# Performance work log

Hardware: AMD Instinct MI355X
Metric: run time of the kernel (lower is better)

The kernel has to match this reference:

```python
import jax, jax.numpy as jnp
import numpy as np

B, C_IN, C_OUT, L = 16, 128, 128, 1024
DK, DV, H = 32, 32, 8
SCALE = DK ** (-0.5)


def setup_inputs() -> dict:
    key = jax.random.key(0)
    ks = jax.random.split(key, 7)
    qkv_dim = H * (2 * DK + DV)
    # Conv1d with kernel_size=1 == per-position linear; store weights as (out, in)
    return {
        "x": jax.random.normal(ks[0], (B, C_IN, L), dtype=jnp.float32),
        "w_qkv": jax.random.normal(ks[1], (qkv_dim, C_IN), dtype=jnp.float32) * (C_IN ** -0.5),
        "b_qkv": jax.random.normal(ks[2], (qkv_dim,), dtype=jnp.float32) * 0.02,
        "w_o": jax.random.normal(ks[3], (C_OUT, H * DV), dtype=jnp.float32) * ((H * DV) ** -0.5),
        "b_o": jax.random.normal(ks[4], (C_OUT,), dtype=jnp.float32) * 0.02,
        "w_res": jax.random.normal(ks[5], (C_OUT, C_IN), dtype=jnp.float32) * (C_IN ** -0.5),
        "b_res": jax.random.normal(ks[6], (C_OUT,), dtype=jnp.float32) * 0.02,
    }


def reference(x, w_qkv, b_qkv, w_o, b_o, w_res, b_res):
    batch, _, seq = x.shape
    # qkv projection (1x1 conv): (B, H*(2dk+dv), L)
    qkv = jnp.einsum("oc,bcl->bol", w_qkv, x) + b_qkv[:, None]
    qkv = qkv.reshape(batch, H, 2 * DK + DV, seq)
    q = qkv[:, :, :DK]                 # (B, H, dk, L)
    k = qkv[:, :, DK:2 * DK]           # (B, H, dk, L)
    v = qkv[:, :, 2 * DK:]             # (B, H, dv, L)
    # logits = scale * q^T k : (B, H, L, L)
    logits = SCALE * jnp.einsum("bhds,bhdt->bhst", q, k)
    weights = jax.nn.softmax(logits, axis=-1)
    # z_i = (weights @ v^T)^T : (B, H, dv, L)
    z = jnp.einsum("bhst,bhdt->bhds", weights, v)
    z = z.reshape(batch, H * DV, seq)
    out = jnp.einsum("oc,bcl->bol", w_o, z) + b_o[:, None]
    out = out + jnp.einsum("oc,bcl->bol", w_res, x) + b_res[:, None]
    return out
```

## Files before the change

kernel.cpp:

```cpp
#include <hip/hip_runtime.h>

#define B_    16
#define L_    1024
#define H_    8
#define QSCALE 0.25510940349191965f

typedef __attribute__((ext_vector_type(8))) short bf16x8;
typedef __attribute__((ext_vector_type(4))) float f32x4;
typedef unsigned short u16t;

__device__ inline u16t f2bf(float f) {
    unsigned u = __float_as_uint(f);
    u = (u + 0x7FFF + ((u >> 16) & 1)) >> 16;
    return (u16t)u;
}
__device__ inline unsigned f2bf_pk(float a, float b) {
    unsigned ua = __float_as_uint(a);
    unsigned ub = __float_as_uint(b);
    ua = (ua + 0x7FFF + ((ua >> 16) & 1)) >> 16;
    ub = (ub + 0x7FFF + ((ub >> 16) & 1)) >> 16;
    return ua | (ub << 16);
}
__device__ inline uint2 f2bf_pk4(float a, float b, float c, float d) {
    uint2 u; u.x = f2bf_pk(a, b); u.y = f2bf_pk(c, d); return u;
}
__device__ inline unsigned trunc_pk(float f0, float f1) {
    return __builtin_amdgcn_perm(__float_as_uint(f1), __float_as_uint(f0), 0x07060302u);
}
__device__ inline void async16(const u16t* g, u16t* l) {
    __builtin_amdgcn_global_load_lds(
        (const __attribute__((address_space(1))) unsigned int*)g,
        (__attribute__((address_space(3))) unsigned int*)l, 16, 0, 0);
}

__global__ __launch_bounds__(256) void prep_kernel(
    const float* __restrict__ x, u16t* __restrict__ xbT)
{
    __shared__ u16t T[64][144];
    const int tid = threadIdx.x;
    const int b = blockIdx.y, l0 = blockIdx.x * 64;
#pragma unroll
    for (int i = 0; i < 8; i++) {
        const int c = i * 16 + (tid >> 4);
        const int l = (tid & 15) * 4;
        const float4 v = *(const float4*)(x + ((long)b * 128 + c) * 1024 + l0 + l);
        T[l + 0][c] = f2bf(v.x);
        T[l + 1][c] = f2bf(v.y);
        T[l + 2][c] = f2bf(v.z);
        T[l + 3][c] = f2bf(v.w);
    }
    __syncthreads();
#pragma unroll
    for (int i = 0; i < 4; i++) {
        const int l  = i * 16 + (tid >> 4);
        const int c0 = (tid & 15) * 8;
        *(uint4*)(xbT + ((long)b * 1024 + l0 + l) * 128 + c0) = *(const uint4*)&T[l][c0];
    }
}

__global__ __launch_bounds__(256) void qkv_gemm_kernel(
    const float* __restrict__ w_qkv, const u16t* __restrict__ xbT,
    const float* __restrict__ b_qkv,
    u16t* __restrict__ qT, u16t* __restrict__ kF, u16t* __restrict__ vF)
{
    __shared__ __align__(16) u16t Ws[96 * 136];

    const int lblk = blockIdx.x * 128;
    const int bh = blockIdx.y;
    const int b = bh >> 3, h = bh & 7;
    const int tid = threadIdx.x, lane = tid & 63, wv = tid >> 6;
    const int l15 = lane & 15, quad = lane >> 4;
    const int lw = lblk + wv * 32;

    {
        const float* wsrc = w_qkv + (long)h * 96 * 128;
#pragma unroll
        for (int it = 0; it < 12; it++) {
            const int g = tid * 4 + it * 1024;
            const int row = g >> 7, col = g & 127;
            const float4 w = *(const float4*)(wsrc + g);
            *(uint2*)&Ws[row * 136 + col] = f2bf_pk4(w.x, w.y, w.z, w.w);
        }
    }

    bf16x8 bfr[4][2];
    {
        const u16t* xr0 = xbT + ((long)b * 1024 + lw + l15) * 128 + quad * 8;
        const u16t* xr1 = xr0 + 16 * 128;
#pragma unroll
        for (int ks = 0; ks < 4; ks++) {
            bfr[ks][0] = *(const bf16x8*)(xr0 + ks * 32);
            bfr[ks][1] = *(const bf16x8*)(xr1 + ks * 32);
        }
    }
    __syncthreads();

    f32x4 acc[6][2];
#pragma unroll
    for (int mi = 0; mi < 6; mi++)
#pragma unroll
        for (int ni = 0; ni < 2; ni++) acc[mi][ni] = (f32x4)0.f;

#pragma unroll
    for (int ks = 0; ks < 4; ks++) {
#pragma unroll
        for (int mi = 0; mi < 6; mi++) {
            const bf16x8 af = *(const bf16x8*)&Ws[(mi * 16 + l15) * 136 + ks * 32 + quad * 8];
            acc[mi][0] = __builtin_amdgcn_mfma_f32_16x16x32_bf16(af, bfr[ks][0], acc[mi][0], 0, 0, 0);
            acc[mi][1] = __builtin_amdgcn_mfma_f32_16x16x32_bf16(af, bfr[ks][1], acc[mi][1], 0, 0, 0);
        }
    }

    const long bh_ = bh;
#pragma unroll
    for (int mi = 0; mi < 6; mi++) {
        float bias[4];
#pragma unroll
        for (int r = 0; r < 4; r++) bias[r] = b_qkv[h * 96 + mi * 16 + quad * 4 + r];
#pragma unroll
        for (int ni = 0; ni < 2; ni++) {
            const int l = lw + ni * 16 + l15;
            const f32x4 a = acc[mi][ni];
            if (mi < 2) {
                const uint2 u = f2bf_pk4((a[0] + bias[0]) * QSCALE, (a[1] + bias[1]) * QSCALE,
                                         (a[2] + bias[2]) * QSCALE, (a[3] + bias[3]) * QSCALE);
                *(uint2*)(qT + (bh_ * 1024 + l) * 32 + mi * 16 + quad * 4) = u;
            } else if (mi < 4) {
                const int t = l, c = t >> 6, tl = t & 63;
                const int qd = (mi - 2) * 2 + (quad >> 1);
                const uint2 u = f2bf_pk4(a[0] + bias[0], a[1] + bias[1],
                                         a[2] + bias[2], a[3] + bias[3]);
                *(uint2*)(kF + (bh_ * 16 + c) * 2048 + qd * 512 + tl * 8 + (quad & 1) * 4) = u;
            } else {
                const int t = l, c = t >> 6, tq = (t >> 3) & 7, j = t & 7;
                u16t* vb = vF + (bh_ * 16 + c) * 2048 + tq * 256 + j;
#pragma unroll
                for (int r = 0; r < 4; r++)
                    vb[((mi - 4) * 16 + quad * 4 + r) * 8] = f2bf(a[r] + bias[r]);
            }
        }
    }
}

__global__ __launch_bounds__(512) void attn_kernel9(
    const u16t* __restrict__ qT, const u16t* __restrict__ kF,
    const u16t* __restrict__ vF, u16t* __restrict__ zT)
{
    __shared__ __align__(16) u16t Ks[2][2048];
    __shared__ __align__(16) u16t Vs[2][2048];
    __shared__ __align__(16) u16t Ps[8][2][2][16][40];

    const int bh = blockIdx.x;
    const int b = bh >> 3, h = bh & 7;
    const int sblk = blockIdx.y * 256;
    const int tid = threadIdx.x, lane = tid & 63, wv = tid >> 6;
    const int l15 = lane & 15, quad = lane >> 4;

    const int sw = sblk + wv * 32;
    bf16x8 qf[2];
    qf[0] = *(const bf16x8*)(qT + ((long)bh * 1024 + sw + l15) * 32 + quad * 8);
    qf[1] = *(const bf16x8*)(qT + ((long)bh * 1024 + sw + 16 + l15) * 32 + quad * 8);

    const u16t* kg = kF + (long)bh * 32768;
    const u16t* vg = vF + (long)bh * 32768;

    if (tid < 256) async16(kg + tid * 8, &Ks[0][tid * 8]);
    else           async16(vg + (tid - 256) * 8, &Vs[0][(tid - 256) * 8]);

    f32x4 zacc[2][2];
#pragma unroll
    for (int a = 0; a < 2; a++)
#pragma unroll
        for (int c = 0; c < 2; c++) zacc[a][c] = (f32x4)0.f;
    f32x4 lacc4[2] = {(f32x4)0.f, (f32x4)0.f};

    for (int c = 0; c < 16; ++c) {
        const int buf = c & 1;
        __syncthreads();
        if (c < 15) {
            const int o = (c + 1) * 2048;
            if (tid < 256) async16(kg + o + tid * 8, &Ks[buf ^ 1][tid * 8]);
            else           async16(vg + o + (tid - 256) * 8, &Vs[buf ^ 1][(tid - 256) * 8]);
        }

        bf16x8 kf[4];
#pragma unroll
        for (int tg = 0; tg < 4; tg++)
            kf[tg] = *(const bf16x8*)&Ks[buf][quad * 512 + (tg * 16 + l15) * 8];

#pragma unroll
        for (int st = 0; st < 2; st++) {
#pragma unroll
            for (int tg = 0; tg < 4; tg++) {
                const f32x4 sv = __builtin_amdgcn_mfma_f32_16x16x32_bf16(kf[tg], qf[st], (f32x4)0.f, 0, 0, 0);
                f32x4 ev;
#pragma unroll
                for (int i = 0; i < 4; i++) ev[i] = __builtin_amdgcn_exp2f(sv[i]);
                lacc4[st] += ev;
                uint2 u;
                u.x = trunc_pk(ev[0], ev[1]);
                u.y = trunc_pk(ev[2], ev[3]);
                *(uint2*)&Ps[wv][st][tg >> 1][l15][(tg & 1) * 16 + quad * 4] = u;
            }
        }

#pragma unroll
        for (int st = 0; st < 2; st++) {
#pragma unroll
            for (int tt = 0; tt < 2; tt++) {
                const bf16x8 pf  = *(const bf16x8*)&Ps[wv][st][tt][l15][quad * 8];
                const bf16x8 vf0 = *(const bf16x8*)&Vs[buf][(tt * 4 + quad) * 256 + l15 * 8];
                const bf16x8 vf1 = *(const bf16x8*)&Vs[buf][(tt * 4 + quad) * 256 + (16 + l15) * 8];
                zacc[st][0] = __builtin_amdgcn_mfma_f32_16x16x32_bf16(vf0, pf, zacc[st][0], 0, 0, 0);
                zacc[st][1] = __builtin_amdgcn_mfma_f32_16x16x32_bf16(vf1, pf, zacc[st][1], 0, 0, 0);
            }
        }
    }

#pragma unroll
    for (int st = 0; st < 2; st++) {
        float lf = (lacc4[st][0] + lacc4[st][1]) + (lacc4[st][2] + lacc4[st][3]);
        lf += __shfl_xor(lf, 16);
        lf += __shfl_xor(lf, 32);
        const float rl = 1.f / lf;
        const int s = sblk + wv * 32 + st * 16 + l15;
        u16t* zrow = zT + ((long)b * 1024 + s) * 256 + h * 32;
        const uint2 u0 = f2bf_pk4(zacc[st][0][0] * rl, zacc[st][0][1] * rl,
                                  zacc[st][0][2] * rl, zacc[st][0][3] * rl);
        *(uint2*)(zrow + quad * 4) = u0;
        const uint2 u1 = f2bf_pk4(zacc[st][1][0] * rl, zacc[st][1][1] * rl,
                                  zacc[st][1][2] * rl, zacc[st][1][3] * rl);
        *(uint2*)(zrow + 16 + quad * 4) = u1;
    }
}

__global__ __launch_bounds__(256) void out_gemm_kernel(
    const float* __restrict__ w_o, const float* __restrict__ w_res,
    const u16t* __restrict__ zT, const u16t* __restrict__ xbT,
    const float* __restrict__ b_o, const float* __restrict__ b_res,
    float* __restrict__ out)
{
    __shared__ __align__(16) u16t Wo[64 * 264];
    __shared__ __align__(16) u16t Wr[64 * 136];

    const int lblk = blockIdx.x * 32, oblk = blockIdx.y * 64, b = blockIdx.z;
    const int tid = threadIdx.x, lane = tid & 63, wv = tid >> 6;
    const int wm = wv >> 1, wn = wv & 1;
    const int l15 = lane & 15, quad = lane >> 4;
    const int ow = oblk + wm * 32;
    const int lw = lblk + wn * 16;

#pragma unroll
    for (int it = 0; it < 16; it++) {
        const int g = tid * 4 + it * 1024;
        const int row = g >> 8, col = g & 255;
        const float4 w = *(const float4*)(w_o + (long)(oblk + row) * 256 + col);
        *(uint2*)&Wo[row * 264 + col] = f2bf_pk4(w.x, w.y, w.z, w.w);
    }
#pragma unroll
    for (int it = 0; it < 8; it++) {
        const int g = tid * 4 + it * 1024;
        const int row = g >> 7, col = g & 127;
        const float4 w = *(const float4*)(w_res + (long)(oblk + row) * 128 + col);
        *(uint2*)&Wr[row * 136 + col] = f2bf_pk4(w.x, w.y, w.z, w.w);
    }

    bf16x8 bfz[8], bfx[4];
    {
        const u16t* zrow = zT + ((long)b * 1024 + lw + l15) * 256 + quad * 8;
        const u16t* xrow = xbT + ((long)b * 1024 + lw + l15) * 128 + quad * 8;
#pragma unroll
        for (int ks = 0; ks < 8; ks++) bfz[ks] = *(const bf16x8*)(zrow + ks * 32);
#pragma unroll
        for (int ks = 0; ks < 4; ks++) bfx[ks] = *(const bf16x8*)(xrow + ks * 32);
    }
    __syncthreads();

    f32x4 acc0 = (f32x4)0.f, acc1 = (f32x4)0.f;

#pragma unroll
    for (int ks = 0; ks < 8; ks++) {
        const bf16x8 af0 = *(const bf16x8*)&Wo[(wm * 32 + l15) * 264 + ks * 32 + quad * 8];
        const bf16x8 af1 = *(const bf16x8*)&Wo[(wm * 32 + 16 + l15) * 264 + ks * 32 + quad * 8];
        acc0 = __builtin_amdgcn_mfma_f32_16x16x32_bf16(af0, bfz[ks], acc0, 0, 0, 0);
        acc1 = __builtin_amdgcn_mfma_f32_16x16x32_bf16(af1, bfz[ks], acc1, 0, 0, 0);
    }
#pragma unroll
    for (int ks = 0; ks < 4; ks++) {
        const bf16x8 af0 = *(const bf16x8*)&Wr[(wm * 32 + l15) * 136 + ks * 32 + quad * 8];
        const bf16x8 af1 = *(const bf16x8*)&Wr[(wm * 32 + 16 + l15) * 136 + ks * 32 + quad * 8];
        acc0 = __builtin_amdgcn_mfma_f32_16x16x32_bf16(af0, bfx[ks], acc0, 0, 0, 0);
        acc1 = __builtin_amdgcn_mfma_f32_16x16x32_bf16(af1, bfx[ks], acc1, 0, 0, 0);
    }

    const int lcol = lw + l15;
#pragma unroll
    for (int mi = 0; mi < 2; mi++) {
        const f32x4 a = (mi == 0) ? acc0 : acc1;
#pragma unroll
        for (int r = 0; r < 4; r++) {
            const int o = ow + mi * 16 + quad * 4 + r;
            out[((long)b * 128 + o) * 1024 + lcol] = a[r] + b_o[o] + b_res[o];
        }
    }
}

extern "C" void kernel_launch(void* const* d_in, const int* in_sizes, int n_in,
                              void* d_out, int out_size, void* d_ws, size_t ws_size,
                              hipStream_t stream)
{
    const float* x     = (const float*)d_in[0];
    const float* w_qkv = (const float*)d_in[1];
    const float* b_qkv = (const float*)d_in[2];
    const float* w_o   = (const float*)d_in[3];
    const float* b_o   = (const float*)d_in[4];
    const float* w_res = (const float*)d_in[5];
    const float* b_res = (const float*)d_in[6];
    float* out = (float*)d_out;

    u16t* xbT = (u16t*)d_ws;
    u16t* qT  = xbT + (size_t)2097152;
    u16t* kF  = qT  + (size_t)4194304;
    u16t* vF  = kF  + (size_t)4194304;
    u16t* zT  = vF  + (size_t)4194304;

    prep_kernel<<<dim3(16, 16), 256, 0, stream>>>(x, xbT);
    qkv_gemm_kernel<<<dim3(8, 128), 256, 0, stream>>>(w_qkv, xbT, b_qkv, qT, kF, vF);
    attn_kernel9<<<dim3(128, 4), 512, 0, stream>>>(qT, kF, vF, zT);
    out_gemm_kernel<<<dim3(32, 2, 16), 256, 0, stream>>>(w_o, w_res, zT, xbT, b_o, b_res, out);
}
```

Measured before the change: 127.0 us.

## Fuse x transpose into QKV GEMM and double attention K/V chunk size

Removes the separate prep kernel. The QKV GEMM now reads fp32 x directly, transposes and converts it into shared memory, and has the h==0 blocks write the bf16 xbT copy the output GEMM still needs. Weights are loaded from global and converted to bf16 per MFMA instead of being staged in LDS. The attention kernel uses 128-key chunks (8 iterations instead of 16), which halves the number of barriers, and the K/V layouts written by the QKV kernel change to match. In exchange, x is reconverted by all 8 head blocks, weight loads become uncoalesced global reads inside the inner loop, and LDS use grows.

```diff
diff --git a/kernel.cpp b/kernel.cpp
--- a/kernel.cpp
+++ b/kernel.cpp
@@ -33,37 +33,13 @@
         (__attribute__((address_space(3))) unsigned int*)l, 16, 0, 0);
 }
 
-__global__ __launch_bounds__(256) void prep_kernel(
-    const float* __restrict__ x, u16t* __restrict__ xbT)
+__global__ __launch_bounds__(256) void qkv_gemm_kernel(
+    const float* __restrict__ w_qkv, const float* __restrict__ x,
+    const float* __restrict__ b_qkv,
+    u16t* __restrict__ qT, u16t* __restrict__ kF, u16t* __restrict__ vF,
+    u16t* __restrict__ xbT)
 {
-    __shared__ u16t T[64][144];
-    const int tid = threadIdx.x;
-    const int b = blockIdx.y, l0 = blockIdx.x * 64;
-#pragma unroll
-    for (int i = 0; i < 8; i++) {
-        const int c = i * 16 + (tid >> 4);
-        const int l = (tid & 15) * 4;
-        const float4 v = *(const float4*)(x + ((long)b * 128 + c) * 1024 + l0 + l);
-        T[l + 0][c] = f2bf(v.x);
-        T[l + 1][c] = f2bf(v.y);
-        T[l + 2][c] = f2bf(v.z);
-        T[l + 3][c] = f2bf(v.w);
-    }
-    __syncthreads();
-#pragma unroll
-    for (int i = 0; i < 4; i++) {
-        const int l  = i * 16 + (tid >> 4);
-        const int c0 = (tid & 15) * 8;
-        *(uint4*)(xbT + ((long)b * 1024 + l0 + l) * 128 + c0) = *(const uint4*)&T[l][c0];
-    }
-}
-
-__global__ __launch_bounds__(256) void qkv_gemm_kernel(
-    const float* __restrict__ w_qkv, const u16t* __restrict__ xbT,
-    const float* __restrict__ b_qkv,
-    u16t* __restrict__ qT, u16t* __restrict__ kF, u16t* __restrict__ vF)
-{
-    __shared__ __align__(16) u16t Ws[96 * 136];
+    __shared__ __align__(16) u16t Xs[128][136];
 
     const int lblk = blockIdx.x * 128;
     const int bh = blockIdx.y;
@@ -72,42 +48,57 @@
     const int l15 = lane & 15, quad = lane >> 4;
     const int lw = lblk + wv * 32;
 
-    {
-        const float* wsrc = w_qkv + (long)h * 96 * 128;
-#pragma unroll
-        for (int it = 0; it < 12; it++) {
-            const int g = tid * 4 + it * 1024;
-            const int row = g >> 7, col = g & 127;
-            const float4 w = *(const float4*)(wsrc + g);
-            *(uint2*)&Ws[row * 136 + col] = f2bf_pk4(w.x, w.y, w.z, w.w);
-        }
-    }
-
-    bf16x8 bfr[4][2];
-    {
-        const u16t* xr0 = xbT + ((long)b * 1024 + lw + l15) * 128 + quad * 8;
-        const u16t* xr1 = xr0 + 16 * 128;
-#pragma unroll
-        for (int ks = 0; ks < 4; ks++) {
-            bfr[ks][0] = *(const bf16x8*)(xr0 + ks * 32);
-            bfr[ks][1] = *(const bf16x8*)(xr1 + ks * 32);
-        }
+#pragma unroll
+    for (int i = 0; i < 8; i++) {
+        const int c  = i * 16 + (tid >> 4);
+        const int l8 = (tid & 15) * 8;
+        const float* xr = x + ((long)b * 128 + c) * 1024 + lblk + l8;
+        const float4 va = *(const float4*)(xr);
+        const float4 vb = *(const float4*)(xr + 4);
+        Xs[l8 + 0][c] = f2bf(va.x);
+        Xs[l8 + 1][c] = f2bf(va.y);
+        Xs[l8 + 2][c] = f2bf(va.z);
+        Xs[l8 + 3][c] = f2bf(va.w);
+        Xs[l8 + 4][c] = f2bf(vb.x);
+        Xs[l8 + 5][c] = f2bf(vb.y);
+        Xs[l8 + 6][c] = f2bf(vb.z);
+        Xs[l8 + 7][c] = f2bf(vb.w);
     }
     __syncthreads();
 
+    if (h == 0) {
+#pragma unroll
+        for (int i = 0; i < 8; i++) {
+            const int l  = i * 16 + (tid >> 4);
+            const int c0 = (tid & 15) * 8;
+            *(uint4*)(xbT + ((long)b * 1024 + lblk + l) * 128 + c0) = *(const uint4*)&Xs[l][c0];
+        }
+    }
+
     f32x4 acc[6][2];
 #pragma unroll
     for (int mi = 0; mi < 6; mi++)
 #pragma unroll
         for (int ni = 0; ni < 2; ni++) acc[mi][ni] = (f32x4)0.f;
 
+    const float* wbase = w_qkv + ((long)h * 96 + l15) * 128 + quad * 8;
+
 #pragma unroll
     for (int ks = 0; ks < 4; ks++) {
+        const bf16x8 bf0 = *(const bf16x8*)&Xs[wv * 32 + l15][ks * 32 + quad * 8];
+        const bf16x8 bf1 = *(const bf16x8*)&Xs[wv * 32 + 16 + l15][ks * 32 + quad * 8];
 #pragma unroll
         for (int mi = 0; mi < 6; mi++) {
-            const bf16x8 af = *(const bf16x8*)&Ws[(mi * 16 + l15) * 136 + ks * 32 + quad * 8];
-            acc[mi][0] = __builtin_amdgcn_mfma_f32_16x16x32_bf16(af, bfr[ks][0], acc[mi][0], 0, 0, 0);
-            acc[mi][1] = __builtin_amdgcn_mfma_f32_16x16x32_bf16(af, bfr[ks][1], acc[mi][1], 0, 0, 0);
+            const float* wr = wbase + mi * 16 * 128 + ks * 32;
+            const float4 wa = *(const float4*)(wr);
+            const float4 wb = *(const float4*)(wr + 4);
+            union { uint4 u; bf16x8 v; } af;
+            af.u.x = f2bf_pk(wa.x, wa.y);
+            af.u.y = f2bf_pk(wa.z, wa.w);
+            af.u.z = f2bf_pk(wb.x, wb.y);
+            af.u.w = f2bf_pk(wb.z, wb.w);
+            acc[mi][0] = __builtin_amdgcn_mfma_f32_16x16x32_bf16(af.v, bf0, acc[mi][0], 0, 0, 0);
+            acc[mi][1] = __builtin_amdgcn_mfma_f32_16x16x32_bf16(af.v, bf1, acc[mi][1], 0, 0, 0);
         }
     }
 
@@ -126,14 +117,14 @@
                                          (a[2] + bias[2]) * QSCALE, (a[3] + bias[3]) * QSCALE);
                 *(uint2*)(qT + (bh_ * 1024 + l) * 32 + mi * 16 + quad * 4) = u;
             } else if (mi < 4) {
-                const int t = l, c = t >> 6, tl = t & 63;
+                const int t = l, c = t >> 7, tl = t & 127;
                 const int qd = (mi - 2) * 2 + (quad >> 1);
                 const uint2 u = f2bf_pk4(a[0] + bias[0], a[1] + bias[1],
                                          a[2] + bias[2], a[3] + bias[3]);
-                *(uint2*)(kF + (bh_ * 16 + c) * 2048 + qd * 512 + tl * 8 + (quad & 1) * 4) = u;
+                *(uint2*)(kF + (bh_ * 8 + c) * 4096 + qd * 1024 + tl * 8 + (quad & 1) * 4) = u;
             } else {
-                const int t = l, c = t >> 6, tq = (t >> 3) & 7, j = t & 7;
-                u16t* vb = vF + (bh_ * 16 + c) * 2048 + tq * 256 + j;
+                const int t = l, c = t >> 7, tq = (t >> 3) & 15, j = t & 7;
+                u16t* vb = vF + (bh_ * 8 + c) * 4096 + tq * 256 + j;
 #pragma unroll
                 for (int r = 0; r < 4; r++)
                     vb[((mi - 4) * 16 + quad * 4 + r) * 8] = f2bf(a[r] + bias[r]);
@@ -142,12 +133,12 @@
     }
 }
 
-__global__ __launch_bounds__(512) void attn_kernel9(
+__global__ __launch_bounds__(512) void attn_kernel10(
     const u16t* __restrict__ qT, const u16t* __restrict__ kF,
     const u16t* __restrict__ vF, u16t* __restrict__ zT)
 {
-    __shared__ __align__(16) u16t Ks[2][2048];
-    __shared__ __align__(16) u16t Vs[2][2048];
+    __shared__ __align__(16) u16t Ks[2][4096];
+    __shared__ __align__(16) u16t Vs[2][4096];
     __shared__ __align__(16) u16t Ps[8][2][2][16][40];
 
     const int bh = blockIdx.x;
@@ -164,8 +155,8 @@
     const u16t* kg = kF + (long)bh * 32768;
     const u16t* vg = vF + (long)bh * 32768;
 
-    if (tid < 256) async16(kg + tid * 8, &Ks[0][tid * 8]);
-    else           async16(vg + (tid - 256) * 8, &Vs[0][(tid - 256) * 8]);
+    async16(kg + tid * 8, &Ks[0][tid * 8]);
+    async16(vg + tid * 8, &Vs[0][tid * 8]);
 
     f32x4 zacc[2][2];
 #pragma unroll
@@ -174,45 +165,49 @@
         for (int c = 0; c < 2; c++) zacc[a][c] = (f32x4)0.f;
     f32x4 lacc4[2] = {(f32x4)0.f, (f32x4)0.f};
 
-    for (int c = 0; c < 16; ++c) {
+    for (int c = 0; c < 8; ++c) {
         const int buf = c & 1;
         __syncthreads();
-        if (c < 15) {
-            const int o = (c + 1) * 2048;
-            if (tid < 256) async16(kg + o + tid * 8, &Ks[buf ^ 1][tid * 8]);
-            else           async16(vg + o + (tid - 256) * 8, &Vs[buf ^ 1][(tid - 256) * 8]);
-        }
-
-        bf16x8 kf[4];
-#pragma unroll
-        for (int tg = 0; tg < 4; tg++)
-            kf[tg] = *(const bf16x8*)&Ks[buf][quad * 512 + (tg * 16 + l15) * 8];
-
-#pragma unroll
-        for (int st = 0; st < 2; st++) {
-#pragma unroll
-            for (int tg = 0; tg < 4; tg++) {
-                const f32x4 sv = __builtin_amdgcn_mfma_f32_16x16x32_bf16(kf[tg], qf[st], (f32x4)0.f, 0, 0, 0);
-                f32x4 ev;
-#pragma unroll
-                for (int i = 0; i < 4; i++) ev[i] = __builtin_amdgcn_exp2f(sv[i]);
-                lacc4[st] += ev;
-                uint2 u;
-                u.x = trunc_pk(ev[0], ev[1]);
-                u.y = trunc_pk(ev[2], ev[3]);
-                *(uint2*)&Ps[wv][st][tg >> 1][l15][(tg & 1) * 16 + quad * 4] = u;
+        if (c < 7) {
+            const int o = (c + 1) * 4096 + tid * 8;
+            async16(kg + o, &Ks[buf ^ 1][tid * 8]);
+            async16(vg + o, &Vs[buf ^ 1][tid * 8]);
+        }
+
+#pragma unroll
+        for (int half = 0; half < 2; half++) {
+            bf16x8 kf[4];
+#pragma unroll
+            for (int tg = 0; tg < 4; tg++)
+                kf[tg] = *(const bf16x8*)&Ks[buf][quad * 1024 + (half * 64 + tg * 16 + l15) * 8];
+
+#pragma unroll
+            for (int st = 0; st < 2; st++) {
+#pragma unroll
+                for (int tg = 0; tg < 4; tg++) {
+                    const f32x4 sv = __builtin_amdgcn_mfma_f32_16x16x32_bf16(kf[tg], qf[st], (f32x4)0.f, 0, 0, 0);
+                    f32x4 ev;
+#pragma unroll
+                    for (int i = 0; i < 4; i++) ev[i] = __builtin_amdgcn_exp2f(sv[i]);
+                    lacc4[st] += ev;
+                    uint2 u;
+                    u.x = trunc_pk(ev[0], ev[1]);
+                    u.y = trunc_pk(ev[2], ev[3]);
+                    *(uint2*)&Ps[wv][st][tg >> 1][l15][(tg & 1) * 16 + quad * 4] = u;
+                }
             }
-        }
-
-#pragma unroll
-        for (int st = 0; st < 2; st++) {
-#pragma unroll
-            for (int tt = 0; tt < 2; tt++) {
-                const bf16x8 pf  = *(const bf16x8*)&Ps[wv][st][tt][l15][quad * 8];
-                const bf16x8 vf0 = *(const bf16x8*)&Vs[buf][(tt * 4 + quad) * 256 + l15 * 8];
-                const bf16x8 vf1 = *(const bf16x8*)&Vs[buf][(tt * 4 + quad) * 256 + (16 + l15) * 8];
-                zacc[st][0] = __builtin_amdgcn_mfma_f32_16x16x32_bf16(vf0, pf, zacc[st][0], 0, 0, 0);
-                zacc[st][1] = __builtin_amdgcn_mfma_f32_16x16x32_bf16(vf1, pf, zacc[st][1], 0, 0, 0);
+
+#pragma unroll
+            for (int st = 0; st < 2; st++) {
+#pragma unroll
+                for (int tt = 0; tt < 2; tt++) {
+                    const int tq = half * 8 + tt * 4 + quad;
+                    const bf16x8 pf  = *(const bf16x8*)&Ps[wv][st][tt][l15][quad * 8];
+                    const bf16x8 vf0 = *(const bf16x8*)&Vs[buf][tq * 256 + l15 * 8];
+                    const bf16x8 vf1 = *(const bf16x8*)&Vs[buf][tq * 256 + (16 + l15) * 8];
+                    zacc[st][0] = __builtin_amdgcn_mfma_f32_16x16x32_bf16(vf0, pf, zacc[st][0], 0, 0, 0);
+                    zacc[st][1] = __builtin_amdgcn_mfma_f32_16x16x32_bf16(vf1, pf, zacc[st][1], 0, 0, 0);
+                }
             }
         }
     }
@@ -324,8 +319,7 @@
     u16t* vF  = kF  + (size_t)4194304;
     u16t* zT  = vF  + (size_t)4194304;
 
-    prep_kernel<<<dim3(16, 16), 256, 0, stream>>>(x, xbT);
-    qkv_gemm_kernel<<<dim3(8, 128), 256, 0, stream>>>(w_qkv, xbT, b_qkv, qT, kF, vF);
-    attn_kernel9<<<dim3(128, 4), 512, 0, stream>>>(qT, kF, vF, zT);
+    qkv_gemm_kernel<<<dim3(8, 128), 256, 0, stream>>>(w_qkv, x, b_qkv, qT, kF, vF, xbT);
+    attn_kernel10<<<dim3(128, 4), 512, 0, stream>>>(qT, kF, vF, zT);
     out_gemm_kernel<<<dim3(32, 2, 16), 256, 0, stream>>>(w_o, w_res, zT, xbT, b_o, b_res, out);
 }
```

New measurement: 144.0 us. 13.4% more time.
